# Optimization experiments

Hardware: AMD Instinct MI355X
Metric: run time of the kernel (lower is better)

## Reference

```python
import jax, jax.numpy as jnp
import numpy as np

B, IN, H = 128, 512, 1024

def setup_inputs() -> dict:
    key = jax.random.key(0)
    ks = jax.random.split(key, 20)
    def lin(kw, kb, out_dim, in_dim):
        lim = 1.0 / np.sqrt(in_dim)
        W = jax.random.uniform(kw, (out_dim, in_dim), minval=-lim, maxval=lim)
        b = jax.random.uniform(kb, (out_dim,), minval=-lim, maxval=lim)
        return W, b
    W1, b1 = lin(ks[0], ks[1], H, IN)
    W2, b2 = lin(ks[2], ks[3], H, H)
    W3, b3 = lin(ks[4], ks[5], H, H)
    Wc, bc = lin(ks[6], ks[7], 1, H)
    Wr, br = lin(ks[8], ks[9], H, 1)
    Wn, bn = lin(ks[10], ks[11], 2, H)
    Wv, bv = lin(ks[12], ks[13], 1, H)
    alpha = 0.01 * (2.0 * jax.random.uniform(ks[14], (H, H)) - 1.0)
    items = jax.random.normal(ks[15], (B, IN))
    plastic_weights = jax.random.normal(ks[16], (B, H, H))
    reward = jax.random.normal(ks[17], (B, 1))
    return dict(items=items, plastic_weights=plastic_weights, reward=reward,
                W1=W1, b1=b1, W2=W2, b2=b2, W3=W3, b3=b3,
                Wc=Wc, bc=bc, Wr=Wr, br=br, Wn=Wn, bn=bn,
                alpha=alpha, Wv=Wv, bv=bv)

def reference(items, plastic_weights, reward, W1, b1, W2, b2, W3, b3,
              Wc, bc, Wr, br, Wn, bn, alpha, Wv, bv):
    # nonlinear item embeddings: [B, H]
    emb = jnp.tanh(items @ W1.T + b1)
    current = emb @ W2.T + b2  # [B, H]
    # elementwise-scaled batched GEMV: (alpha * plastic)[b,h,i] @ emb[b,i]
    plastic_contrib = jnp.einsum('bhi,bi->bh', alpha * plastic_weights, emb)
    pre_tanh_hidden = current + plastic_contrib
    hidden = jnp.tanh(pre_tanh_hidden)
    reward_emb = reward @ Wr.T + br  # [B, H]
    nm_out = jnp.tanh((jnp.tanh((hidden + reward_emb) @ W3.T + b3)) @ Wn.T + bn)  # [B, 2]
    neuromodulator = (nm_out[:, 0] - nm_out[:, 1])[:, None, None]  # [B,1,1]
    choice = jax.nn.sigmoid(hidden @ Wc.T + bc)  # [B, 1]
    value = hidden @ Wv.T + bv  # [B, 1]
    # Hebbian outer-product trace: [B, H, H]
    hebbian = jnp.tanh(jnp.einsum('bh,bi->bhi', pre_tanh_hidden, emb)) * 10.0
    new_plastic = jnp.clip(plastic_weights + neuromodulator * hebbian, -50.0, 50.0)
    return (choice, neuromodulator, value, new_plastic, hidden)
```

## Files before the change

kernel.cpp:

```cpp
#include <hip/hip_runtime.h>
#include <hip/hip_bf16.h>

#define BATCH 128
#define IN_DIM 512
#define HDIM 1024
#define CHUNK 16
#define K2_BCHUNK 4
#define K3_BCHUNK 8

typedef __attribute__((ext_vector_type(4))) float f32x4;

__device__ __forceinline__ float fast_tanh(float x) {
    float e = __expf(2.0f * x);
    return 1.0f - 2.0f * __builtin_amdgcn_rcpf(e + 1.0f);
}

__global__ __launch_bounds__(256) void k1_emb(
    const float* __restrict__ items, const float* __restrict__ W1,
    const float* __restrict__ b1, const float* __restrict__ bn,
    float* __restrict__ emb_f, float* __restrict__ nm_acc)
{
    __shared__ float it[IN_DIM];
    int b = blockIdx.x, t = threadIdx.x;
    if (b == 0) nm_acc[t] = bn[t & 1];
    it[t] = items[b * IN_DIM + t];
    it[t + 256] = items[b * IN_DIM + t + 256];
    __syncthreads();
    #pragma unroll
    for (int j = 0; j < 4; ++j) {
        int h = t + 256 * j;
        const float* wrow = W1 + h * IN_DIM;
        float acc = 0.f;
        #pragma unroll 4
        for (int c = 0; c < IN_DIM; c += 4) {
            f32x4 w = *reinterpret_cast<const f32x4*>(wrow + c);
            acc += w[0] * it[c] + w[1] * it[c + 1] + w[2] * it[c + 2] + w[3] * it[c + 3];
        }
        emb_f[b * HDIM + h] = tanhf(acc + b1[h]);
    }
}

__global__ __launch_bounds__(256) void k2_hidden(
    const float* __restrict__ plastic, const float* __restrict__ alpha,
    const float* __restrict__ W2, const float* __restrict__ b2,
    const float* __restrict__ emb_f, float* __restrict__ pre_f,
    float* __restrict__ hid_f, int b0)
{
    int hg = blockIdx.x & 255;
    int bg = blockIdx.x >> 8;
    int w  = threadIdx.x >> 6;
    int l  = threadIdx.x & 63;
    int h  = (hg << 2) + w;

    const float* arow = alpha + (h << 10);
    const float* wrow = W2 + (h << 10);
    f32x4 ar[4], wr[4];
    #pragma unroll
    for (int c = 0; c < 4; ++c) {
        int i = c * 256 + l * 4;
        ar[c] = *reinterpret_cast<const f32x4*>(arow + i);
        wr[c] = *reinterpret_cast<const f32x4*>(wrow + i);
    }
    float b2h = b2[h];

    #pragma unroll 2
    for (int bb = 0; bb < K2_BCHUNK; ++bb) {
        int b = b0 + bg * K2_BCHUNK + bb;
        const float* prow = plastic + (((size_t)b) << 20) + ((size_t)h << 10);
        const float* erow = emb_f + (b << 10);
        float acc = 0.f;
        #pragma unroll
        for (int c = 0; c < 4; ++c) {
            int i = c * 256 + l * 4;
            f32x4 p = *reinterpret_cast<const f32x4*>(prow + i);
            f32x4 e = *reinterpret_cast<const f32x4*>(erow + i);
            acc += e[0] * fmaf(ar[c][0], p[0], wr[c][0]);
            acc += e[1] * fmaf(ar[c][1], p[1], wr[c][1]);
            acc += e[2] * fmaf(ar[c][2], p[2], wr[c][2]);
            acc += e[3] * fmaf(ar[c][3], p[3], wr[c][3]);
        }
        #pragma unroll
        for (int off = 32; off > 0; off >>= 1) acc += __shfl_xor(acc, off);
        if (l == 0) {
            float pre = acc + b2h;
            pre_f[(b << 10) + h] = pre;
            hid_f[(b << 10) + h] = tanhf(pre);
        }
    }
}

__global__ __launch_bounds__(256) void k3a_nm(
    const float* __restrict__ hid_f, const float* __restrict__ reward,
    const float* __restrict__ Wr, const float* __restrict__ br,
    const float* __restrict__ W3, const float* __restrict__ b3,
    const float* __restrict__ Wn, float* __restrict__ nm_acc, int b0)
{
    int hg = blockIdx.x & 255;
    int bg = blockIdx.x >> 8;
    int w  = threadIdx.x >> 6;
    int l  = threadIdx.x & 63;
    int h  = (hg << 2) + w;

    const float* wrow = W3 + (h << 10);
    f32x4 w3r[4], wrr[4], brr[4];
    #pragma unroll
    for (int c = 0; c < 4; ++c) {
        int i = c * 256 + l * 4;
        w3r[c] = *reinterpret_cast<const f32x4*>(wrow + i);
        wrr[c] = *reinterpret_cast<const f32x4*>(Wr + i);
        brr[c] = *reinterpret_cast<const f32x4*>(br + i);
    }
    float b3h = b3[h];
    float wn0 = Wn[h], wn1 = Wn[HDIM + h];

    __shared__ float part[4][K3_BCHUNK][2];

    for (int bb = 0; bb < K3_BCHUNK; ++bb) {
        int b = b0 + bg * K3_BCHUNK + bb;
        float rw = reward[b];
        const float* hrow = hid_f + (b << 10);
        float acc = 0.f;
        #pragma unroll
        for (int c = 0; c < 4; ++c) {
            int i = c * 256 + l * 4;
            f32x4 hh = *reinterpret_cast<const f32x4*>(hrow + i);
            #pragma unroll
            for (int j = 0; j < 4; ++j)
                acc += (hh[j] + fmaf(rw, wrr[c][j], brr[c][j])) * w3r[c][j];
        }
        #pragma unroll
        for (int off = 32; off > 0; off >>= 1) acc += __shfl_xor(acc, off);
        if (l == 0) {
            float t3 = tanhf(acc + b3h);
            part[w][bb][0] = t3 * wn0;
            part[w][bb][1] = t3 * wn1;
        }
    }
    __syncthreads();
    int t = threadIdx.x;
    if (t < K3_BCHUNK * 2) {
        int bb = t >> 1, j = t & 1;
        float s = part[0][bb][j] + part[1][bb][j] + part[2][bb][j] + part[3][bb][j];
        atomicAdd(nm_acc + ((b0 + bg * K3_BCHUNK + bb) << 1) + j, s);
    }
}

__global__ __launch_bounds__(256) void k4_update(
    const float* __restrict__ plastic, const float* __restrict__ emb_f,
    const float* __restrict__ pre_f, const float* __restrict__ nm_acc,
    float* __restrict__ outp, int b0)
{
    size_t idx = (((size_t)b0) << 20) + ((size_t)blockIdx.x * 256 + threadIdx.x) * 4;
    int b   = (int)(idx >> 20);
    int rem = (int)(idx & 1048575u);
    int h   = rem >> 10;
    int i0  = rem & 1023;
    float nm  = fast_tanh(nm_acc[2 * b]) - fast_tanh(nm_acc[2 * b + 1]);
    float pre = pre_f[(b << 10) + h];
    f32x4 p = __builtin_nontemporal_load(reinterpret_cast<const f32x4*>(plastic + idx));
    f32x4 e = *reinterpret_cast<const f32x4*>(emb_f + (b << 10) + i0);
    f32x4 o;
    #pragma unroll
    for (int j = 0; j < 4; ++j) {
        float heb = fast_tanh(pre * e[j]) * 10.0f;
        float v = fmaf(nm, heb, p[j]);
        o[j] = fminf(fmaxf(v, -50.0f), 50.0f);
    }
    __builtin_nontemporal_store(o, reinterpret_cast<f32x4*>(outp + idx));
}

__global__ __launch_bounds__(256) void k3c_heads(
    const float* __restrict__ hid_f, const float* __restrict__ nm_acc,
    const float* __restrict__ Wc, const float* __restrict__ bc,
    const float* __restrict__ Wv, const float* __restrict__ bv,
    float* __restrict__ out)
{
    int b = blockIdx.x, t = threadIdx.x;
    int w = t >> 6, l = t & 63;
    const float* hrow = hid_f + (b << 10);
    if (w < 2) {
        const float* wv = (w == 0) ? Wc : Wv;
        float acc = 0.f;
        #pragma unroll
        for (int c = 0; c < 4; ++c) {
            int i = c * 256 + l * 4;
            f32x4 wg = *reinterpret_cast<const f32x4*>(wv + i);
            f32x4 ss = *reinterpret_cast<const f32x4*>(hrow + i);
            acc += ss[0] * wg[0] + ss[1] * wg[1] + ss[2] * wg[2] + ss[3] * wg[3];
        }
        #pragma unroll
        for (int off = 32; off > 0; off >>= 1) acc += __shfl_xor(acc, off);
        if (l == 0) {
            if (w == 0) out[b] = 1.0f / (1.0f + __expf(-(acc + bc[0])));
            else        out[2 * BATCH + b] = acc + bv[0];
        }
    } else if (t == 128) {
        out[BATCH + b] = tanhf(nm_acc[2 * b]) - tanhf(nm_acc[2 * b + 1]);
    }
    const size_t HID_OFF = (size_t)3 * BATCH + (size_t)BATCH * HDIM * HDIM;
    for (int i = t; i < HDIM; i += 256)
        out[HID_OFF + (size_t)b * HDIM + i] = hrow[i];
}

extern "C" void kernel_launch(void* const* d_in, const int* in_sizes, int n_in,
                              void* d_out, int out_size, void* d_ws, size_t ws_size,
                              hipStream_t stream)
{
    const float* items   = (const float*)d_in[0];
    const float* plastic = (const float*)d_in[1];
    const float* reward  = (const float*)d_in[2];
    const float* W1 = (const float*)d_in[3];
    const float* b1 = (const float*)d_in[4];
    const float* W2 = (const float*)d_in[5];
    const float* b2 = (const float*)d_in[6];
    const float* W3 = (const float*)d_in[7];
    const float* b3 = (const float*)d_in[8];
    const float* Wc = (const float*)d_in[9];
    const float* bc = (const float*)d_in[10];
    const float* Wr = (const float*)d_in[11];
    const float* br = (const float*)d_in[12];
    const float* Wn = (const float*)d_in[13];
    const float* bn = (const float*)d_in[14];
    const float* alpha = (const float*)d_in[15];
    const float* Wv = (const float*)d_in[16];
    const float* bv = (const float*)d_in[17];

    float* ws     = (float*)d_ws;
    float* emb_f  = ws;
    float* pre_f  = ws + 131072;
    float* hid_f  = ws + 262144;
    float* nm_acc = ws + 393216;

    float* out  = (float*)d_out;
    float* outp = out + 384;

    k1_emb<<<BATCH, 256, 0, stream>>>(items, W1, b1, bn, emb_f, nm_acc);

    for (int b0 = 0; b0 < BATCH; b0 += CHUNK) {
        k2_hidden<<<256 * (CHUNK / K2_BCHUNK), 256, 0, stream>>>(
            plastic, alpha, W2, b2, emb_f, pre_f, hid_f, b0);
        k3a_nm<<<256 * (CHUNK / K3_BCHUNK), 256, 0, stream>>>(
            hid_f, reward, Wr, br, W3, b3, Wn, nm_acc, b0);
        k4_update<<<(CHUNK << 20) / 1024, 256, 0, stream>>>(
            plastic, emb_f, pre_f, nm_acc, outp, b0);
    }

    k3c_heads<<<BATCH, 256, 0, stream>>>(hid_f, nm_acc, Wc, bc, Wv, bv, out);
}
```

Measured before the change: 441.2 us.

## Replace chunked batch loop with single launches and reverse-order update traversal

Removes the 16-batch chunking loop so each of k2, k3a and k4 launches once over the whole batch. The chunks were sized so the plastic slice read by k2 could still be in cache when k4 read it again. k4 now walks blocks in reverse order so the most recently streamed plastic rows are hit first while still cached. It also switches plastic loads from nontemporal to normal loads, processes 8 floats per thread, and doubles the k2 batch chunk. The trade is fewer launches against possibly weaker cache reuse of the 512MB plastic tensor between k2 and k4.

```diff
diff --git a/kernel.cpp b/kernel.cpp
--- a/kernel.cpp
+++ b/kernel.cpp
@@ -4,8 +4,7 @@
 #define BATCH 128
 #define IN_DIM 512
 #define HDIM 1024
-#define CHUNK 16
-#define K2_BCHUNK 4
+#define K2_BCHUNK 8
 #define K3_BCHUNK 8
 
 typedef __attribute__((ext_vector_type(4))) float f32x4;
@@ -44,7 +43,7 @@
     const float* __restrict__ plastic, const float* __restrict__ alpha,
     const float* __restrict__ W2, const float* __restrict__ b2,
     const float* __restrict__ emb_f, float* __restrict__ pre_f,
-    float* __restrict__ hid_f, int b0)
+    float* __restrict__ hid_f)
 {
     int hg = blockIdx.x & 255;
     int bg = blockIdx.x >> 8;
@@ -65,7 +64,7 @@
 
     #pragma unroll 2
     for (int bb = 0; bb < K2_BCHUNK; ++bb) {
-        int b = b0 + bg * K2_BCHUNK + bb;
+        int b = bg * K2_BCHUNK + bb;
         const float* prow = plastic + (((size_t)b) << 20) + ((size_t)h << 10);
         const float* erow = emb_f + (b << 10);
         float acc = 0.f;
@@ -93,7 +92,7 @@
     const float* __restrict__ hid_f, const float* __restrict__ reward,
     const float* __restrict__ Wr, const float* __restrict__ br,
     const float* __restrict__ W3, const float* __restrict__ b3,
-    const float* __restrict__ Wn, float* __restrict__ nm_acc, int b0)
+    const float* __restrict__ Wn, float* __restrict__ nm_acc)
 {
     int hg = blockIdx.x & 255;
     int bg = blockIdx.x >> 8;
@@ -116,7 +115,7 @@
     __shared__ float part[4][K3_BCHUNK][2];
 
     for (int bb = 0; bb < K3_BCHUNK; ++bb) {
-        int b = b0 + bg * K3_BCHUNK + bb;
+        int b = bg * K3_BCHUNK + bb;
         float rw = reward[b];
         const float* hrow = hid_f + (b << 10);
         float acc = 0.f;
@@ -141,32 +140,37 @@
     if (t < K3_BCHUNK * 2) {
         int bb = t >> 1, j = t & 1;
         float s = part[0][bb][j] + part[1][bb][j] + part[2][bb][j] + part[3][bb][j];
-        atomicAdd(nm_acc + ((b0 + bg * K3_BCHUNK + bb) << 1) + j, s);
+        atomicAdd(nm_acc + ((bg * K3_BCHUNK + bb) << 1) + j, s);
     }
 }
 
 __global__ __launch_bounds__(256) void k4_update(
     const float* __restrict__ plastic, const float* __restrict__ emb_f,
     const float* __restrict__ pre_f, const float* __restrict__ nm_acc,
-    float* __restrict__ outp, int b0)
-{
-    size_t idx = (((size_t)b0) << 20) + ((size_t)blockIdx.x * 256 + threadIdx.x) * 4;
+    float* __restrict__ outp)
+{
+    const int NBLK = (int)(((size_t)BATCH << 20) / 2048);
+    size_t idx = ((size_t)(NBLK - 1 - blockIdx.x)) * 2048 + (size_t)threadIdx.x * 8;
     int b   = (int)(idx >> 20);
     int rem = (int)(idx & 1048575u);
     int h   = rem >> 10;
     int i0  = rem & 1023;
     float nm  = fast_tanh(nm_acc[2 * b]) - fast_tanh(nm_acc[2 * b + 1]);
     float pre = pre_f[(b << 10) + h];
-    f32x4 p = __builtin_nontemporal_load(reinterpret_cast<const f32x4*>(plastic + idx));
-    f32x4 e = *reinterpret_cast<const f32x4*>(emb_f + (b << 10) + i0);
-    f32x4 o;
+    f32x4 p0 = *reinterpret_cast<const f32x4*>(plastic + idx);
+    f32x4 p1 = *reinterpret_cast<const f32x4*>(plastic + idx + 4);
+    f32x4 e0 = *reinterpret_cast<const f32x4*>(emb_f + (b << 10) + i0);
+    f32x4 e1 = *reinterpret_cast<const f32x4*>(emb_f + (b << 10) + i0 + 4);
+    f32x4 o0, o1;
     #pragma unroll
     for (int j = 0; j < 4; ++j) {
-        float heb = fast_tanh(pre * e[j]) * 10.0f;
-        float v = fmaf(nm, heb, p[j]);
-        o[j] = fminf(fmaxf(v, -50.0f), 50.0f);
-    }
-    __builtin_nontemporal_store(o, reinterpret_cast<f32x4*>(outp + idx));
+        float v0 = fmaf(nm, fast_tanh(pre * e0[j]) * 10.0f, p0[j]);
+        float v1 = fmaf(nm, fast_tanh(pre * e1[j]) * 10.0f, p1[j]);
+        o0[j] = fminf(fmaxf(v0, -50.0f), 50.0f);
+        o1[j] = fminf(fmaxf(v1, -50.0f), 50.0f);
+    }
+    __builtin_nontemporal_store(o0, reinterpret_cast<f32x4*>(outp + idx));
+    __builtin_nontemporal_store(o1, reinterpret_cast<f32x4*>(outp + idx + 4));
 }
 
 __global__ __launch_bounds__(256) void k3c_heads(
@@ -234,16 +238,12 @@
     float* out  = (float*)d_out;
     float* outp = out + 384;
 
-    k1_emb<<<BATCH, 256, 0, stream>>>(items, W1, b1, bn, emb_f, nm_acc);
-
-    for (int b0 = 0; b0 < BATCH; b0 += CHUNK) {
-        k2_hidden<<<256 * (CHUNK / K2_BCHUNK), 256, 0, stream>>>(
-            plastic, alpha, W2, b2, emb_f, pre_f, hid_f, b0);
-        k3a_nm<<<256 * (CHUNK / K3_BCHUNK), 256, 0, stream>>>(
-            hid_f, reward, Wr, br, W3, b3, Wn, nm_acc, b0);
-        k4_update<<<(CHUNK << 20) / 1024, 256, 0, stream>>>(
-            plastic, emb_f, pre_f, nm_acc, outp, b0);
-    }
-
+    k1_emb   <<<BATCH, 256, 0, stream>>>(items, W1, b1, bn, emb_f, nm_acc);
+    k2_hidden<<<256 * (BATCH / K2_BCHUNK), 256, 0, stream>>>(
+        plastic, alpha, W2, b2, emb_f, pre_f, hid_f);
+    k3a_nm   <<<256 * (BATCH / K3_BCHUNK), 256, 0, stream>>>(
+        hid_f, reward, Wr, br, W3, b3, Wn, nm_acc);
+    k4_update<<<(int)(((size_t)BATCH << 20) / 2048), 256, 0, stream>>>(
+        plastic, emb_f, pre_f, nm_acc, outp);
     k3c_heads<<<BATCH, 256, 0, stream>>>(hid_f, nm_acc, Wc, bc, Wv, bv, out);
 }
```

After: 404.5 us. -8.3%, faster.
